# Kernel tuning notes

Measured on AMD Instinct MI355X. Metric: run time of the kernel, lower is better.

Reference implementation:

```python
import jax, jax.numpy as jnp
import numpy as np

N = 8192
IN_F = 512
OUT_F = 256
POW = 2


def setup_inputs() -> dict:
    key = jax.random.key(0)
    k1, k2, k3, k4 = jax.random.split(key, 4)
    stdv = 1.0 / np.sqrt(OUT_F)
    inputs = {
        "input": jax.random.normal(k1, (N, IN_F), dtype=jnp.float32),
        "adj": jax.random.uniform(k2, (N, N), dtype=jnp.float32),
        "weight": jax.random.uniform(k3, (IN_F, OUT_F), dtype=jnp.float32, minval=-stdv, maxval=stdv),
        "bias": jax.random.uniform(k4, (OUT_F,), dtype=jnp.float32, minval=-stdv, maxval=stdv),
    }
    return inputs


def reference(input, adj, weight, bias):
    # K_adj = adj ** pow (elementwise power, as torch's ** on a dense tensor)
    k_adj = adj ** POW
    # support = X @ W  -> [N, out_features]
    support = jnp.einsum("ni,io->no", input, weight)
    # output = K_adj @ support -> [N, out_features]
    out = jnp.einsum("nm,mo->no", k_adj, support) + bias
    # F.elu with default alpha=1.0
    return jnp.where(out > 0, out, jnp.expm1(out))
```

## Files before the change

kernel.cpp:

```cpp
#include <hip/hip_runtime.h>
#include <cstdint>
#include <cstddef>

#define N_NODES 8192
#define INF 512
#define OUTF 256

typedef _Float16 f16;
typedef _Float16 f16x8 __attribute__((ext_vector_type(8)));
typedef float f32x4 __attribute__((ext_vector_type(4)));

__device__ __forceinline__ void async_copy16(void* lds_dst, const void* g_src) {
  __builtin_amdgcn_global_load_lds(
      (const __attribute__((address_space(1))) void*)g_src,
      (__attribute__((address_space(3))) void*)lds_dst,
      16, 0, 0);
}

__global__ __launch_bounds__(256) void gemm1_xw(
    const float* __restrict__ X, const float* __restrict__ W,
    f16* __restrict__ supT) {
  __shared__ __align__(16) f16 Asm[64][72];
  __shared__ __align__(16) f16 Bsm[128][72];
  const int t = threadIdx.x;
  const int wave = t >> 6;
  const int lane = t & 63;
  const int q = lane >> 4;
  const int r = lane & 15;
  const int o0 = blockIdx.x * 64;
  const int m0 = blockIdx.y * 128;

  f32x4 acc[4][2];
#pragma unroll
  for (int i = 0; i < 4; ++i)
#pragma unroll
    for (int j = 0; j < 2; ++j)
      acc[i][j] = (f32x4){0.f, 0.f, 0.f, 0.f};

  const int a_o = t & 63;
  const int a_i = (t >> 6) * 16;
  const int b_m = t >> 1;
  const int b_i = (t & 1) * 32;
  const float* xrow = X + (size_t)(m0 + b_m) * INF + b_i;

  for (int kt = 0; kt < 8; ++kt) {
    const int k0 = kt * 64;
    {
      f16x8 h0, h1;
#pragma unroll
      for (int u = 0; u < 8; ++u)
        h0[u] = (f16)W[(size_t)(k0 + a_i + u) * OUTF + o0 + a_o];
#pragma unroll
      for (int u = 0; u < 8; ++u)
        h1[u] = (f16)W[(size_t)(k0 + a_i + 8 + u) * OUTF + o0 + a_o];
      *(f16x8*)&Asm[a_o][a_i] = h0;
      *(f16x8*)&Asm[a_o][a_i + 8] = h1;
    }
    {
      const float* xp = xrow + k0;
#pragma unroll
      for (int c = 0; c < 4; ++c) {
        f32x4 v0 = *(const f32x4*)(xp + c * 8);
        f32x4 v1 = *(const f32x4*)(xp + c * 8 + 4);
        f16x8 h;
#pragma unroll
        for (int u = 0; u < 4; ++u) {
          h[u] = (f16)v0[u];
          h[4 + u] = (f16)v1[u];
        }
        *(f16x8*)&Bsm[b_m][b_i + c * 8] = h;
      }
    }
    __syncthreads();
#pragma unroll
    for (int s = 0; s < 2; ++s) {
      f16x8 af[4], bf[2];
#pragma unroll
      for (int i = 0; i < 4; ++i)
        af[i] = *(const f16x8*)&Asm[i * 16 + r][s * 32 + q * 8];
#pragma unroll
      for (int j = 0; j < 2; ++j)
        bf[j] = *(const f16x8*)&Bsm[wave * 32 + j * 16 + r][s * 32 + q * 8];
#pragma unroll
      for (int i = 0; i < 4; ++i)
#pragma unroll
        for (int j = 0; j < 2; ++j)
          acc[i][j] = __builtin_amdgcn_mfma_f32_16x16x32_f16(af[i], bf[j],
                                                             acc[i][j], 0, 0, 0);
    }
    __syncthreads();
  }
#pragma unroll
  for (int i = 0; i < 4; ++i) {
#pragma unroll
    for (int j = 0; j < 2; ++j) {
      const int m = m0 + wave * 32 + j * 16 + r;
#pragma unroll
      for (int g = 0; g < 4; ++g) {
        const int o = o0 + i * 16 + q * 4 + g;
        supT[(size_t)o * N_NODES + m] = (f16)acc[i][j][g];
      }
    }
  }
}

__global__ __launch_bounds__(256) void gemm2_adj(
    const float* __restrict__ adj, const f16* __restrict__ supT,
    float* __restrict__ out) {
  __shared__ __align__(16) f16 Asm[64][72];
  __shared__ __align__(16) f16 Bsm[256 * 64];
  const int t = threadIdx.x;
  const int wave = t >> 6;
  const int lane = t & 63;
  const int q = lane >> 4;
  const int r = lane & 15;
  const int n0 = blockIdx.x * 64;
  const size_t m_base = (size_t)blockIdx.y * 4096;

  f32x4 acc[4][4];
#pragma unroll
  for (int i = 0; i < 4; ++i)
#pragma unroll
    for (int j = 0; j < 4; ++j)
      acc[i][j] = (f32x4){0.f, 0.f, 0.f, 0.f};

  const int a_row = t >> 2;
  const int a_col = (t & 3) * 16;
  const float* aptr = adj + (size_t)(n0 + a_row) * N_NODES + m_base + a_col;

  const int b_o = wave * 64 + (lane >> 3);
  const int b_kb = lane & 7;

  for (int kt = 0; kt < 64; ++kt) {
#pragma unroll
    for (int j = 0; j < 8; ++j) {
      const int o = b_o + j * 8;
      const int kb = b_kb ^ (o & 7);
      const f16* src = supT + (size_t)o * N_NODES + m_base + kt * 64 + kb * 8;
      f16* dst = Bsm + (wave * 64 + j * 8) * 64;
      async_copy16(dst, src);
    }
    {
      const float* ap = aptr + kt * 64;
      f32x4 v0 = *(const f32x4*)(ap + 0);
      f32x4 v1 = *(const f32x4*)(ap + 4);
      f32x4 v2 = *(const f32x4*)(ap + 8);
      f32x4 v3 = *(const f32x4*)(ap + 12);
      f16x8 h0, h1;
#pragma unroll
      for (int u = 0; u < 4; ++u) {
        h0[u] = (f16)(v0[u] * v0[u]);
        h0[4 + u] = (f16)(v1[u] * v1[u]);
        h1[u] = (f16)(v2[u] * v2[u]);
        h1[4 + u] = (f16)(v3[u] * v3[u]);
      }
      *(f16x8*)&Asm[a_row][a_col] = h0;
      *(f16x8*)&Asm[a_row][a_col + 8] = h1;
    }
    __syncthreads();
#pragma unroll
    for (int s = 0; s < 2; ++s) {
      f16x8 af[4], bf[4];
#pragma unroll
      for (int i = 0; i < 4; ++i)
        af[i] = *(const f16x8*)&Asm[i * 16 + r][s * 32 + q * 8];
#pragma unroll
      for (int j = 0; j < 4; ++j) {
        const int o = wave * 64 + j * 16 + r;
        const int cc = (s * 4 + q) ^ (r & 7);
        bf[j] = *(const f16x8*)&Bsm[o * 64 + cc * 8];
      }
#pragma unroll
      for (int i = 0; i < 4; ++i)
#pragma unroll
        for (int j = 0; j < 4; ++j)
          acc[i][j] = __builtin_amdgcn_mfma_f32_16x16x32_f16(af[i], bf[j],
                                                             acc[i][j], 0, 0, 0);
    }
    __syncthreads();
  }
#pragma unroll
  for (int i = 0; i < 4; ++i) {
#pragma unroll
    for (int g = 0; g < 4; ++g) {
      const int n = n0 + i * 16 + q * 4 + g;
      float* orow = out + (size_t)n * OUTF + wave * 64 + r;
#pragma unroll
      for (int j = 0; j < 4; ++j)
        atomicAdd(orow + j * 16, acc[i][j][g]);
    }
  }
}

__global__ __launch_bounds__(256) void bias_elu(float* __restrict__ out,
                                                const float* __restrict__ bias) {
  const int idx = blockIdx.x * 256 + threadIdx.x;
  f32x4 v = ((const f32x4*)out)[idx];
  const f32x4 b = ((const f32x4*)bias)[idx & 63];
#pragma unroll
  for (int u = 0; u < 4; ++u) {
    const float x = v[u] + b[u];
    v[u] = x > 0.f ? x : expm1f(x);
  }
  ((f32x4*)out)[idx] = v;
}

extern "C" void kernel_launch(void* const* d_in, const int* in_sizes, int n_in,
                              void* d_out, int out_size, void* d_ws, size_t ws_size,
                              hipStream_t stream) {
  const float* X = (const float*)d_in[0];
  const float* adj = (const float*)d_in[1];
  const float* W = (const float*)d_in[2];
  const float* bias = (const float*)d_in[3];
  float* out = (float*)d_out;
  f16* supT = (f16*)d_ws;

  hipMemsetAsync(d_out, 0, (size_t)out_size * sizeof(float), stream);
  gemm1_xw<<<dim3(4, 64), 256, 0, stream>>>(X, W, supT);
  gemm2_adj<<<dim3(128, 2), 256, 0, stream>>>(adj, supT, out);
  bias_elu<<<out_size / 1024, 256, 0, stream>>>(out, bias);
}
```

Before: 450.6 us.

## Split gemm2 over eight K slices with partial buffers and fused reduce-ELU

The adjacency GEMM split-K factor rises from 2 to 8, giving 1024 blocks instead of 256 so more CUs are busy. When workspace allows, each slice writes its own partial buffer and a fused reduce+bias+ELU kernel sums them, replacing atomics and the memset. GEMM1 now uses pre-cast fp16 X and a pre-transposed fp16 W loaded via async LDS copies with XOR swizzle, and gemm2's A tile is swizzled too. This adds extra kernels and roughly 64 MB of partial-sum traffic, and needs 80 MB of workspace for the non-atomic path.

```diff
diff --git a/kernel.cpp b/kernel.cpp
--- a/kernel.cpp
+++ b/kernel.cpp
@@ -5,6 +5,8 @@
 #define N_NODES 8192
 #define INF 512
 #define OUTF 256
+#define SPLITK 8
+#define MSLICE (N_NODES / SPLITK)
 
 typedef _Float16 f16;
 typedef _Float16 f16x8 __attribute__((ext_vector_type(8)));
@@ -17,70 +19,70 @@
       16, 0, 0);
 }
 
-__global__ __launch_bounds__(256) void gemm1_xw(
-    const float* __restrict__ X, const float* __restrict__ W,
-    f16* __restrict__ supT) {
-  __shared__ __align__(16) f16 Asm[64][72];
-  __shared__ __align__(16) f16 Bsm[128][72];
+__device__ __forceinline__ float elu(float x) { return x > 0.f ? x : expm1f(x); }
+
+__global__ __launch_bounds__(256) void cast_x(const float* __restrict__ X,
+                                              f16* __restrict__ Xh) {
+  const int idx = blockIdx.x * 256 + threadIdx.x;
+  f32x4 v0 = ((const f32x4*)X)[idx * 2];
+  f32x4 v1 = ((const f32x4*)X)[idx * 2 + 1];
+  f16x8 h;
+#pragma unroll
+  for (int u = 0; u < 4; ++u) {
+    h[u] = (f16)v0[u];
+    h[4 + u] = (f16)v1[u];
+  }
+  ((f16x8*)Xh)[idx] = h;
+}
+
+__global__ __launch_bounds__(256) void transpose_w(const float* __restrict__ W,
+                                                   f16* __restrict__ WhT) {
+  const int idx = blockIdx.x * 256 + threadIdx.x;
+  const int o = idx >> 9, i = idx & 511;
+  WhT[idx] = (f16)W[i * OUTF + o];
+}
+
+__global__ __launch_bounds__(256) void gemm1(const f16* __restrict__ WhT,
+                                             const f16* __restrict__ Xh,
+                                             f16* __restrict__ supT) {
+  __shared__ __align__(16) f16 Asm[64 * 64];
+  __shared__ __align__(16) f16 Bsm[128 * 64];
   const int t = threadIdx.x;
-  const int wave = t >> 6;
-  const int lane = t & 63;
-  const int q = lane >> 4;
-  const int r = lane & 15;
-  const int o0 = blockIdx.x * 64;
-  const int m0 = blockIdx.y * 128;
+  const int wave = t >> 6, lane = t & 63;
+  const int q = lane >> 4, r = lane & 15;
+  const int lrow = lane >> 3, lchunk = lane & 7;
+  const int o0 = blockIdx.x * 64, m0 = blockIdx.y * 128;
 
   f32x4 acc[4][2];
 #pragma unroll
   for (int i = 0; i < 4; ++i)
 #pragma unroll
-    for (int j = 0; j < 2; ++j)
-      acc[i][j] = (f32x4){0.f, 0.f, 0.f, 0.f};
-
-  const int a_o = t & 63;
-  const int a_i = (t >> 6) * 16;
-  const int b_m = t >> 1;
-  const int b_i = (t & 1) * 32;
-  const float* xrow = X + (size_t)(m0 + b_m) * INF + b_i;
+    for (int j = 0; j < 2; ++j) acc[i][j] = (f32x4){0.f, 0.f, 0.f, 0.f};
 
   for (int kt = 0; kt < 8; ++kt) {
     const int k0 = kt * 64;
-    {
-      f16x8 h0, h1;
-#pragma unroll
-      for (int u = 0; u < 8; ++u)
-        h0[u] = (f16)W[(size_t)(k0 + a_i + u) * OUTF + o0 + a_o];
-#pragma unroll
-      for (int u = 0; u < 8; ++u)
-        h1[u] = (f16)W[(size_t)(k0 + a_i + 8 + u) * OUTF + o0 + a_o];
-      *(f16x8*)&Asm[a_o][a_i] = h0;
-      *(f16x8*)&Asm[a_o][a_i + 8] = h1;
-    }
-    {
-      const float* xp = xrow + k0;
-#pragma unroll
-      for (int c = 0; c < 4; ++c) {
-        f32x4 v0 = *(const f32x4*)(xp + c * 8);
-        f32x4 v1 = *(const f32x4*)(xp + c * 8 + 4);
-        f16x8 h;
-#pragma unroll
-        for (int u = 0; u < 4; ++u) {
-          h[u] = (f16)v0[u];
-          h[4 + u] = (f16)v1[u];
-        }
-        *(f16x8*)&Bsm[b_m][b_i + c * 8] = h;
-      }
+#pragma unroll
+    for (int op = 0; op < 2; ++op) {
+      const int row = (wave * 2 + op) * 8 + lrow;
+      const f16* src = WhT + (size_t)(o0 + row) * INF + k0 + (lchunk ^ lrow) * 8;
+      async_copy16(Asm + (wave * 2 + op) * 8 * 64, src);
+    }
+#pragma unroll
+    for (int op = 0; op < 4; ++op) {
+      const int row = (wave * 4 + op) * 8 + lrow;
+      const f16* src = Xh + (size_t)(m0 + row) * INF + k0 + (lchunk ^ lrow) * 8;
+      async_copy16(Bsm + (wave * 4 + op) * 8 * 64, src);
     }
     __syncthreads();
 #pragma unroll
     for (int s = 0; s < 2; ++s) {
+      const int pc = ((s * 4 + q) ^ (r & 7)) * 8;
       f16x8 af[4], bf[2];
 #pragma unroll
-      for (int i = 0; i < 4; ++i)
-        af[i] = *(const f16x8*)&Asm[i * 16 + r][s * 32 + q * 8];
+      for (int i = 0; i < 4; ++i) af[i] = *(const f16x8*)&Asm[(i * 16 + r) * 64 + pc];
 #pragma unroll
       for (int j = 0; j < 2; ++j)
-        bf[j] = *(const f16x8*)&Bsm[wave * 32 + j * 16 + r][s * 32 + q * 8];
+        bf[j] = *(const f16x8*)&Bsm[(wave * 32 + j * 16 + r) * 64 + pc];
 #pragma unroll
       for (int i = 0; i < 4; ++i)
 #pragma unroll
@@ -91,54 +93,47 @@
     __syncthreads();
   }
 #pragma unroll
-  for (int i = 0; i < 4; ++i) {
+  for (int i = 0; i < 4; ++i)
 #pragma unroll
     for (int j = 0; j < 2; ++j) {
       const int m = m0 + wave * 32 + j * 16 + r;
 #pragma unroll
-      for (int g = 0; g < 4; ++g) {
-        const int o = o0 + i * 16 + q * 4 + g;
-        supT[(size_t)o * N_NODES + m] = (f16)acc[i][j][g];
-      }
-    }
-  }
-}
-
-__global__ __launch_bounds__(256) void gemm2_adj(
-    const float* __restrict__ adj, const f16* __restrict__ supT,
-    float* __restrict__ out) {
-  __shared__ __align__(16) f16 Asm[64][72];
+      for (int g = 0; g < 4; ++g)
+        supT[(size_t)(o0 + i * 16 + q * 4 + g) * N_NODES + m] = (f16)acc[i][j][g];
+    }
+}
+
+template <bool ATOMIC>
+__global__ __launch_bounds__(256, 4) void gemm2(const float* __restrict__ adj,
+                                                const f16* __restrict__ supT,
+                                                float* __restrict__ outp) {
+  __shared__ __align__(16) f16 Asm[64 * 64];
   __shared__ __align__(16) f16 Bsm[256 * 64];
   const int t = threadIdx.x;
-  const int wave = t >> 6;
-  const int lane = t & 63;
-  const int q = lane >> 4;
-  const int r = lane & 15;
+  const int wave = t >> 6, lane = t & 63;
+  const int q = lane >> 4, r = lane & 15;
   const int n0 = blockIdx.x * 64;
-  const size_t m_base = (size_t)blockIdx.y * 4096;
+  const size_t m_base = (size_t)blockIdx.y * MSLICE;
 
   f32x4 acc[4][4];
 #pragma unroll
   for (int i = 0; i < 4; ++i)
 #pragma unroll
-    for (int j = 0; j < 4; ++j)
-      acc[i][j] = (f32x4){0.f, 0.f, 0.f, 0.f};
+    for (int j = 0; j < 4; ++j) acc[i][j] = (f32x4){0.f, 0.f, 0.f, 0.f};
 
   const int a_row = t >> 2;
-  const int a_col = (t & 3) * 16;
-  const float* aptr = adj + (size_t)(n0 + a_row) * N_NODES + m_base + a_col;
-
+  const int a_c0 = (t & 3) * 2;
+  const float* aptr = adj + (size_t)(n0 + a_row) * N_NODES + m_base + (t & 3) * 16;
   const int b_o = wave * 64 + (lane >> 3);
   const int b_kb = lane & 7;
 
-  for (int kt = 0; kt < 64; ++kt) {
+  for (int kt = 0; kt < MSLICE / 64; ++kt) {
 #pragma unroll
     for (int j = 0; j < 8; ++j) {
       const int o = b_o + j * 8;
       const int kb = b_kb ^ (o & 7);
       const f16* src = supT + (size_t)o * N_NODES + m_base + kt * 64 + kb * 8;
-      f16* dst = Bsm + (wave * 64 + j * 8) * 64;
-      async_copy16(dst, src);
+      async_copy16(Bsm + (wave * 64 + j * 8) * 64, src);
     }
     {
       const float* ap = aptr + kt * 64;
@@ -154,22 +149,19 @@
         h1[u] = (f16)(v2[u] * v2[u]);
         h1[4 + u] = (f16)(v3[u] * v3[u]);
       }
-      *(f16x8*)&Asm[a_row][a_col] = h0;
-      *(f16x8*)&Asm[a_row][a_col + 8] = h1;
+      *(f16x8*)&Asm[a_row * 64 + ((a_c0 ^ (a_row & 7)) * 8)] = h0;
+      *(f16x8*)&Asm[a_row * 64 + (((a_c0 + 1) ^ (a_row & 7)) * 8)] = h1;
     }
     __syncthreads();
 #pragma unroll
     for (int s = 0; s < 2; ++s) {
+      const int pc = ((s * 4 + q) ^ (r & 7)) * 8;
       f16x8 af[4], bf[4];
 #pragma unroll
-      for (int i = 0; i < 4; ++i)
-        af[i] = *(const f16x8*)&Asm[i * 16 + r][s * 32 + q * 8];
-#pragma unroll
-      for (int j = 0; j < 4; ++j) {
-        const int o = wave * 64 + j * 16 + r;
-        const int cc = (s * 4 + q) ^ (r & 7);
-        bf[j] = *(const f16x8*)&Bsm[o * 64 + cc * 8];
-      }
+      for (int i = 0; i < 4; ++i) af[i] = *(const f16x8*)&Asm[(i * 16 + r) * 64 + pc];
+#pragma unroll
+      for (int j = 0; j < 4; ++j)
+        bf[j] = *(const f16x8*)&Bsm[(wave * 64 + j * 16 + r) * 64 + pc];
 #pragma unroll
       for (int i = 0; i < 4; ++i)
 #pragma unroll
@@ -179,17 +171,36 @@
     }
     __syncthreads();
   }
-#pragma unroll
-  for (int i = 0; i < 4; ++i) {
+  float* base = ATOMIC ? outp : outp + (size_t)blockIdx.y * N_NODES * OUTF;
+#pragma unroll
+  for (int i = 0; i < 4; ++i)
 #pragma unroll
     for (int g = 0; g < 4; ++g) {
       const int n = n0 + i * 16 + q * 4 + g;
-      float* orow = out + (size_t)n * OUTF + wave * 64 + r;
-#pragma unroll
-      for (int j = 0; j < 4; ++j)
-        atomicAdd(orow + j * 16, acc[i][j][g]);
-    }
-  }
+      float* orow = base + (size_t)n * OUTF + wave * 64 + r;
+#pragma unroll
+      for (int j = 0; j < 4; ++j) {
+        if (ATOMIC)
+          atomicAdd(orow + j * 16, acc[i][j][g]);
+        else
+          orow[j * 16] = acc[i][j][g];
+      }
+    }
+}
+
+__global__ __launch_bounds__(256) void reduce_elu(const float* __restrict__ P,
+                                                  const float* __restrict__ bias,
+                                                  float* __restrict__ out) {
+  const int idx = blockIdx.x * 256 + threadIdx.x;
+  f32x4 s = (f32x4){0.f, 0.f, 0.f, 0.f};
+#pragma unroll
+  for (int y = 0; y < SPLITK; ++y)
+    s += ((const f32x4*)(P + (size_t)y * N_NODES * OUTF))[idx];
+  const f32x4 b = ((const f32x4*)bias)[idx & 63];
+  f32x4 v;
+#pragma unroll
+  for (int u = 0; u < 4; ++u) v[u] = elu(s[u] + b[u]);
+  ((f32x4*)out)[idx] = v;
 }
 
 __global__ __launch_bounds__(256) void bias_elu(float* __restrict__ out,
@@ -198,10 +209,7 @@
   f32x4 v = ((const f32x4*)out)[idx];
   const f32x4 b = ((const f32x4*)bias)[idx & 63];
 #pragma unroll
-  for (int u = 0; u < 4; ++u) {
-    const float x = v[u] + b[u];
-    v[u] = x > 0.f ? x : expm1f(x);
-  }
+  for (int u = 0; u < 4; ++u) v[u] = elu(v[u] + b[u]);
   ((f32x4*)out)[idx] = v;
 }
 
@@ -213,10 +221,23 @@
   const float* W = (const float*)d_in[2];
   const float* bias = (const float*)d_in[3];
   float* out = (float*)d_out;
-  f16* supT = (f16*)d_ws;
-
-  hipMemsetAsync(d_out, 0, (size_t)out_size * sizeof(float), stream);
-  gemm1_xw<<<dim3(4, 64), 256, 0, stream>>>(X, W, supT);
-  gemm2_adj<<<dim3(128, 2), 256, 0, stream>>>(adj, supT, out);
-  bias_elu<<<out_size / 1024, 256, 0, stream>>>(out, bias);
-}
+
+  char* ws = (char*)d_ws;
+  f16* supT = (f16*)(ws + 0);
+  f16* Xh = (f16*)(ws + (4u << 20));
+  f16* WhT = (f16*)(ws + (12u << 20));
+  float* P = (float*)(ws + (16u << 20));
+  const size_t need = (80u << 20);
+
+  cast_x<<<N_NODES * INF / 8 / 256, 256, 0, stream>>>(X, Xh);
+  transpose_w<<<INF * OUTF / 256, 256, 0, stream>>>(W, WhT);
+  gemm1<<<dim3(OUTF / 64, N_NODES / 128), 256, 0, stream>>>(WhT, Xh, supT);
+  if (ws_size >= need) {
+    gemm2<false><<<dim3(N_NODES / 64, SPLITK), 256, 0, stream>>>(adj, supT, P);
+    reduce_elu<<<N_NODES * OUTF / 4 / 256, 256, 0, stream>>>(P, bias, out);
+  } else {
+    hipMemsetAsync(d_out, 0, (size_t)out_size * sizeof(float), stream);
+    gemm2<true><<<dim3(N_NODES / 64, SPLITK), 256, 0, stream>>>(adj, supT, out);
+    bias_elu<<<N_NODES * OUTF / 4 / 256, 256, 0, stream>>>(out, bias);
+  }
+}
```

New measurement: 443.4 us. Within noise of the previous version (-1.6%).
